# Kernel tuning notes

Measured on AMD Instinct MI355X. Metric: run time of the kernel, lower is better.

Reference implementation:

```python
import jax, jax.numpy as jnp
import numpy as np

BUF = 4096   # buffer_size (sliding window)
B, H, S, D = 4, 8, 512, 128  # batch, kv heads, new seq chunk, head_dim
CUR_LEN = 6144  # current_seq_len > BUF so scatter and gather both wrap


def setup_inputs() -> dict:
    key = jax.random.key(0)
    k0, k1, k2, k3 = jax.random.split(key, 4)
    return {
        "k": jax.random.normal(k0, (B, H, S, D), dtype=jnp.float32),
        "v": jax.random.normal(k1, (B, H, S, D), dtype=jnp.float32),
        "k_cache": jax.random.normal(k2, (B, H, BUF, D), dtype=jnp.float32),
        "v_cache": jax.random.normal(k3, (B, H, BUF, D), dtype=jnp.float32),
        "current_seq_len": CUR_LEN,
    }


def reference(k, v, k_cache, v_cache, current_seq_len):
    batch, num_heads, seq_len, head_dim = k.shape
    buf = k_cache.shape[2]
    # circular-buffer scatter of the new chunk
    start_idx = (current_seq_len - seq_len) % buf
    cache_idx = (start_idx + jnp.arange(seq_len)) % buf  # [S]
    k_cache = k_cache.at[:, :, cache_idx].set(k)
    v_cache = v_cache.at[:, :, cache_idx].set(v)
    # gather the logical sliding window in temporal order
    window = min(current_seq_len, buf)  # static Python int
    phys = jnp.arange(current_seq_len - window, current_seq_len) % buf  # [W]
    k_window = jnp.take(k_cache, phys, axis=2)  # [B,H,W,D]
    v_window = jnp.take(v_cache, phys, axis=2)
    return k_window, v_window
```

## Files before the change

### kernel.cpp

```cpp
#include <hip/hip_runtime.h>


constexpr int Bc   = 4;
constexpr int Hc   = 8;
constexpr int Sc   = 512;
constexpr int Dc   = 128;
constexpr int BUFc = 4096;
constexpr int D4   = Dc / 4;
constexpr int Wc   = BUFc;

__global__ __launch_bounds__(256)
void RollingBufferCache_kernel(const float4* __restrict__ kn,
                               const float4* __restrict__ vn,
                               const float4* __restrict__ kc,
                               const float4* __restrict__ vc,
                               const int*    __restrict__ curp,
                               float4*       __restrict__ out)
{
    const int cur       = *curp;
    const int window    = (cur < Wc) ? cur : Wc;
    const int start_w   = cur - window;
    const int start_idx = (cur - Sc) & (BUFc - 1);

    const long half   = (long)Bc * Hc * Wc * D4;
    const long total  = 2 * half;
    const long stride = (long)gridDim.x * blockDim.x;

    for (long i = (long)blockIdx.x * blockDim.x + threadIdx.x; i < total; i += stride) {
        const bool is_v = (i >= half);
        const long j    = is_v ? (i - half) : i;

        const int d4 = (int)(j & (D4 - 1));
        const int t  = (int)((j >> 5) & (Wc - 1));
        const int bh = (int)(j >> 17);

        const int p   = (start_w + t) & (BUFc - 1);
        const int off = (p - start_idx) & (BUFc - 1);

        float4 val;
        if (off < Sc) {
            const float4* __restrict__ src = is_v ? vn : kn;
            val = src[((long)bh * Sc + off) * D4 + d4];
        } else {
            const float4* __restrict__ src = is_v ? vc : kc;
            val = src[((long)bh * BUFc + p) * D4 + d4];
        }
        out[i] = val;
    }
}

extern "C" void kernel_launch(void* const* d_in, const int* in_sizes, int n_in,
                              void* d_out, int out_size, void* d_ws, size_t ws_size,
                              hipStream_t stream) {
    const float4* kn   = (const float4*)d_in[0];
    const float4* vn   = (const float4*)d_in[1];
    const float4* kc   = (const float4*)d_in[2];
    const float4* vc   = (const float4*)d_in[3];
    const int*    curp = (const int*)  d_in[4];
    float4*       out  = (float4*)     d_out;

    RollingBufferCache_kernel<<<2048, 256, 0, stream>>>(kn, vn, kc, vc, curp, out);
}
```

Measured before the change: 247.0 us.

## Unroll gather with paired K/V loads, exact grid and nontemporal stores

Replaces the grid-stride loop with an exact-cover grid where each thread handles four positions and loads both K and V for each before storing. All loads are issued ahead of the stores to raise memory-level parallelism. Stores use nontemporal hints to avoid polluting cache. Index math moves to 32-bit ints, and the launch grid grows from a fixed 2048 blocks to the exact cover.

```diff
diff --git a/kernel.cpp b/kernel.cpp
--- a/kernel.cpp
+++ b/kernel.cpp
@@ -1,5 +1,7 @@
 #include <hip/hip_runtime.h>
 
+
+typedef float fvec4 __attribute__((ext_vector_type(4)));
 
 constexpr int Bc   = 4;
 constexpr int Hc   = 8;
@@ -8,56 +10,71 @@
 constexpr int BUFc = 4096;
 constexpr int D4   = Dc / 4;
 constexpr int Wc   = BUFc;
+constexpr int HALF = Bc * Hc * Wc * D4;
+constexpr int UNROLL = 4;
+constexpr int THREADS = 256;
+constexpr int GRID = HALF / (THREADS * UNROLL);
 
-__global__ __launch_bounds__(256)
-void RollingBufferCache_kernel(const float4* __restrict__ kn,
-                               const float4* __restrict__ vn,
-                               const float4* __restrict__ kc,
-                               const float4* __restrict__ vc,
-                               const int*    __restrict__ curp,
-                               float4*       __restrict__ out)
+static_assert(GRID * THREADS * UNROLL == HALF, "exact grid cover");
+
+__global__ __launch_bounds__(THREADS)
+void RollingBufferCache_kernel(const fvec4* __restrict__ kn,
+                               const fvec4* __restrict__ vn,
+                               const fvec4* __restrict__ kc,
+                               const fvec4* __restrict__ vc,
+                               const int*   __restrict__ curp,
+                               fvec4*       __restrict__ out)
 {
     const int cur       = *curp;
     const int window    = (cur < Wc) ? cur : Wc;
     const int start_w   = cur - window;
     const int start_idx = (cur - Sc) & (BUFc - 1);
 
-    const long half   = (long)Bc * Hc * Wc * D4;
-    const long total  = 2 * half;
-    const long stride = (long)gridDim.x * blockDim.x;
+    const int base = blockIdx.x * (THREADS * UNROLL) + threadIdx.x;
 
-    for (long i = (long)blockIdx.x * blockDim.x + threadIdx.x; i < total; i += stride) {
-        const bool is_v = (i >= half);
-        const long j    = is_v ? (i - half) : i;
+    fvec4 kv[UNROLL];
+    fvec4 vv[UNROLL];
+    int   oj[UNROLL];
 
-        const int d4 = (int)(j & (D4 - 1));
-        const int t  = (int)((j >> 5) & (Wc - 1));
-        const int bh = (int)(j >> 17);
+    #pragma unroll
+    for (int u = 0; u < UNROLL; ++u) {
+        const int j  = base + u * THREADS;
+        const int d4 = j & (D4 - 1);
+        const int t  = (j >> 5) & (Wc - 1);
+        const int bh = j >> 17;
 
         const int p   = (start_w + t) & (BUFc - 1);
         const int off = (p - start_idx) & (BUFc - 1);
+        const bool in_new = (off < Sc);
 
-        float4 val;
-        if (off < Sc) {
-            const float4* __restrict__ src = is_v ? vn : kn;
-            val = src[((long)bh * Sc + off) * D4 + d4];
-        } else {
-            const float4* __restrict__ src = is_v ? vc : kc;
-            val = src[((long)bh * BUFc + p) * D4 + d4];
-        }
-        out[i] = val;
+        const int cj = (bh << 17) + (p << 5) + d4;
+        const int nj = (bh << 14) + (off << 5) + d4;
+
+        const fvec4* __restrict__ sk = in_new ? kn : kc;
+        const fvec4* __restrict__ sv = in_new ? vn : vc;
+        const int o = in_new ? nj : cj;
+
+        kv[u] = sk[o];
+        vv[u] = sv[o];
+        oj[u] = j;
+    }
+
+    #pragma unroll
+    for (int u = 0; u < UNROLL; ++u) {
+        __builtin_nontemporal_store(kv[u], &out[oj[u]]);
+        __builtin_nontemporal_store(vv[u], &out[HALF + oj[u]]);
     }
 }
 
 extern "C" void kernel_launch(void* const* d_in, const int* in_sizes, int n_in,
                               void* d_out, int out_size, void* d_ws, size_t ws_size,
                               hipStream_t stream) {
-    const float4* kn   = (const float4*)d_in[0];
-    const float4* vn   = (const float4*)d_in[1];
-    const float4* kc   = (const float4*)d_in[2];
-    const float4* vc   = (const float4*)d_in[3];
-    const int*    curp = (const int*)  d_in[4];
-    float4*       out  = (float4*)     d_out;
+    const fvec4* kn   = (const fvec4*)d_in[0];
+    const fvec4* vn   = (const fvec4*)d_in[1];
+    const fvec4* kc   = (const fvec4*)d_in[2];
+    const fvec4* vc   = (const fvec4*)d_in[3];
+    const int*   curp = (const int*) d_in[4];
+    fvec4*       out  = (fvec4*)     d_out;
 
-    RollingBufferCache_kernel<<<2048, 256, 0, stream>>>(kn, vn, kc, vc, curp, out);
+    RollingBufferCache_kernel<<<GRID, THREADS, 0, stream>>>(kn, vn, kc, vc, curp, out);
 }
```

Measured after the change: 248.1 us. No clear change (+0.4%).
